# Optimization experiments

Hardware: AMD Instinct MI355X
Metric: run time of the kernel (lower is better)

## Reference

```python
import jax, jax.numpy as jnp
import numpy as np

B, W, F, N = 256, 512, 512, 512


def setup_inputs() -> dict:
    key = jax.random.key(0)
    k1, k2, k3, k4, k5 = jax.random.split(key, 5)
    return {
        "x": jax.random.normal(k1, (B, W, F), dtype=jnp.float32),
        "weight_k": jax.random.normal(k2, (F, N), dtype=jnp.float32),
        "weight_q": jax.random.normal(k3, (F, N), dtype=jnp.float32),
        "weight_v": jax.random.normal(k4, (F, N), dtype=jnp.float32),
        "w": jax.random.normal(k5, (W, 1), dtype=jnp.float32),
    }


def reference(x, weight_k, weight_q, weight_v, w):
    # x: (B, W, F)
    n_outputs = weight_k.shape[-1]
    # Per-word K/V projections (original loops over words; here one batched GEMM)
    K = jnp.einsum("bwf,fn->bwn", x, weight_k)  # (B, W, N)
    V = jnp.einsum("bwf,fn->bwn", x, weight_v)  # (B, W, N)
    # Per-sample query: t = x^T @ w -> (F,), q = t @ weight_q -> (N,)
    t = jnp.einsum("bwf,w->bf", x, w[:, 0])     # (B, F)
    Q = t @ weight_q                              # (B, N)
    # Scores over words, scaled, softmax across the word axis
    scores = jnp.einsum("bn,bwn->bw", Q, K) / jnp.sqrt(jnp.float32(n_outputs))
    weights = jax.nn.softmax(scores, axis=1)      # (B, W)
    # Weighted sum of V over words
    return jnp.einsum("bw,bwn->bn", weights, V)   # (B, N)
```

## Files before the change

kernel.cpp:

```cpp
#include <hip/hip_runtime.h>
#include <math.h>

#define B 256
#define W 512
#define F 512
#define N 512
#define GP 8
#define WPB (W / GP)

__global__ __launch_bounds__(256, 8) void tpart_kernel(
    const float* __restrict__ x,
    const float* __restrict__ wvec,
    float* __restrict__ t_part)
{
    const int blk  = blockIdx.x;
    const int g    = blk & (GP - 1);
    const int b    = blk >> 3;
    const int tid  = threadIdx.x;
    const int half = tid >> 7;
    const int f4   = tid & 127;

    __shared__ float s_w[WPB];
    __shared__ float s_part[2][F];

    if (tid < WPB) s_w[tid] = wvec[g * WPB + tid];
    __syncthreads();

    const float* xb = x + (size_t)b * W * F + (size_t)(g * WPB + half * 32) * F;
    float4 acc = make_float4(0.f, 0.f, 0.f, 0.f);
#pragma unroll 8
    for (int i = 0; i < 32; ++i) {
        const float4 xv = *(const float4*)(xb + (size_t)i * F + f4 * 4);
        const float  ww = s_w[half * 32 + i];
        acc.x += xv.x * ww; acc.y += xv.y * ww;
        acc.z += xv.z * ww; acc.w += xv.w * ww;
    }
    *(float4*)&s_part[half][f4 * 4] = acc;
    __syncthreads();

    t_part[(size_t)blk * F + tid]       = s_part[0][tid]       + s_part[1][tid];
    t_part[(size_t)blk * F + tid + 256] = s_part[0][tid + 256] + s_part[1][tid + 256];
}

__global__ __launch_bounds__(512) void qr_kernel(
    const float* __restrict__ t_part,
    const float* __restrict__ Wq,
    const float* __restrict__ Wk,
    float* __restrict__ r_out)
{
    __shared__ float s_t[F];
    __shared__ float s_q[N];
    const int b = blockIdx.x, tid = threadIdx.x;

    float t = 0.f;
#pragma unroll
    for (int g = 0; g < GP; ++g)
        t += t_part[((size_t)b * GP + g) * F + tid];
    s_t[tid] = t;
    __syncthreads();

    float qa[8] = {0.f, 0.f, 0.f, 0.f, 0.f, 0.f, 0.f, 0.f};
#pragma unroll 4
    for (int f = 0; f < F; f += 8) {
#pragma unroll
        for (int j = 0; j < 8; ++j)
            qa[j] += s_t[f + j] * Wq[(size_t)(f + j) * N + tid];
    }
    s_q[tid] = ((qa[0] + qa[1]) + (qa[2] + qa[3]))
             + ((qa[4] + qa[5]) + (qa[6] + qa[7]));
    __syncthreads();

    const float4* wkrow = (const float4*)(Wk + (size_t)tid * N);
    float r0 = 0.f, r1 = 0.f, r2 = 0.f, r3 = 0.f;
#pragma unroll 8
    for (int n4 = 0; n4 < N / 4; ++n4) {
        const float4 kv = wkrow[n4];
        const float4 qv = *(const float4*)&s_q[n4 * 4];
        r0 += kv.x * qv.x; r1 += kv.y * qv.y;
        r2 += kv.z * qv.z; r3 += kv.w * qv.w;
    }
    r_out[(size_t)b * F + tid] =
        ((r0 + r1) + (r2 + r3)) * 0.04419417382415922f;
}

__global__ __launch_bounds__(256) void attn_part_kernel(
    const float* __restrict__ x,
    const float* __restrict__ r_in,
    float* __restrict__ c_part,
    float* __restrict__ ml_part)
{
    const int blk  = blockIdx.x;
    const int g    = blk & (GP - 1);
    const int b    = blk >> 3;
    const int tid  = threadIdx.x;
    const int lane = tid & 63;
    const int wv   = tid >> 6;

    __shared__ float s_c[4][F];
    __shared__ float s_m[4];
    __shared__ float s_l[4];

    const float* xb = x + (size_t)b * W * F;
    const float* rb = r_in + (size_t)b * F;
    const float4 r0 = *(const float4*)(rb + lane * 4);
    const float4 r1 = *(const float4*)(rb + 256 + lane * 4);

    float m0 = -INFINITY, l0 = 0.f, m1 = -INFINITY, l1 = 0.f;
    float4 cA0 = make_float4(0.f,0.f,0.f,0.f), cA1 = make_float4(0.f,0.f,0.f,0.f);
    float4 cB0 = make_float4(0.f,0.f,0.f,0.f), cB1 = make_float4(0.f,0.f,0.f,0.f);

    const int wbase = g * WPB + wv * 16;
    for (int i = 0; i < 16; i += 4) {
        const float* rA = xb + (size_t)(wbase + i) * F;
        const float* rB = rA + F;
        const float* rC = rB + F;
        const float* rD = rC + F;
        const float4 a0 = *(const float4*)(rA + lane * 4);
        const float4 a1 = *(const float4*)(rA + 256 + lane * 4);
        const float4 b0 = *(const float4*)(rB + lane * 4);
        const float4 b1 = *(const float4*)(rB + 256 + lane * 4);
        const float4 e0 = *(const float4*)(rC + lane * 4);
        const float4 e1 = *(const float4*)(rC + 256 + lane * 4);
        const float4 f0 = *(const float4*)(rD + lane * 4);
        const float4 f1 = *(const float4*)(rD + 256 + lane * 4);

        float dA = a0.x*r0.x + a0.y*r0.y + a0.z*r0.z + a0.w*r0.w
                 + a1.x*r1.x + a1.y*r1.y + a1.z*r1.z + a1.w*r1.w;
        float dB = b0.x*r0.x + b0.y*r0.y + b0.z*r0.z + b0.w*r0.w
                 + b1.x*r1.x + b1.y*r1.y + b1.z*r1.z + b1.w*r1.w;
        float dC = e0.x*r0.x + e0.y*r0.y + e0.z*r0.z + e0.w*r0.w
                 + e1.x*r1.x + e1.y*r1.y + e1.z*r1.z + e1.w*r1.w;
        float dD = f0.x*r0.x + f0.y*r0.y + f0.z*r0.z + f0.w*r0.w
                 + f1.x*r1.x + f1.y*r1.y + f1.z*r1.z + f1.w*r1.w;
#pragma unroll
        for (int off = 32; off >= 1; off >>= 1) {
            dA += __shfl_xor(dA, off, 64);
            dB += __shfl_xor(dB, off, 64);
            dC += __shfl_xor(dC, off, 64);
            dD += __shfl_xor(dD, off, 64);
        }

        {
            float mn = fmaxf(m0, dA);
            float sc = __expf(m0 - mn);
            float p  = __expf(dA - mn);
            l0 = l0 * sc + p;
            cA0.x = cA0.x*sc + p*a0.x; cA0.y = cA0.y*sc + p*a0.y;
            cA0.z = cA0.z*sc + p*a0.z; cA0.w = cA0.w*sc + p*a0.w;
            cA1.x = cA1.x*sc + p*a1.x; cA1.y = cA1.y*sc + p*a1.y;
            cA1.z = cA1.z*sc + p*a1.z; cA1.w = cA1.w*sc + p*a1.w;
            m0 = mn;
            mn = fmaxf(m0, dB);
            sc = __expf(m0 - mn);
            p  = __expf(dB - mn);
            l0 = l0 * sc + p;
            cA0.x = cA0.x*sc + p*b0.x; cA0.y = cA0.y*sc + p*b0.y;
            cA0.z = cA0.z*sc + p*b0.z; cA0.w = cA0.w*sc + p*b0.w;
            cA1.x = cA1.x*sc + p*b1.x; cA1.y = cA1.y*sc + p*b1.y;
            cA1.z = cA1.z*sc + p*b1.z; cA1.w = cA1.w*sc + p*b1.w;
            m0 = mn;
        }
        {
            float mn = fmaxf(m1, dC);
            float sc = __expf(m1 - mn);
            float p  = __expf(dC - mn);
            l1 = l1 * sc + p;
            cB0.x = cB0.x*sc + p*e0.x; cB0.y = cB0.y*sc + p*e0.y;
            cB0.z = cB0.z*sc + p*e0.z; cB0.w = cB0.w*sc + p*e0.w;
            cB1.x = cB1.x*sc + p*e1.x; cB1.y = cB1.y*sc + p*e1.y;
            cB1.z = cB1.z*sc + p*e1.z; cB1.w = cB1.w*sc + p*e1.w;
            m1 = mn;
            mn = fmaxf(m1, dD);
            sc = __expf(m1 - mn);
            p  = __expf(dD - mn);
            l1 = l1 * sc + p;
            cB0.x = cB0.x*sc + p*f0.x; cB0.y = cB0.y*sc + p*f0.y;
            cB0.z = cB0.z*sc + p*f0.z; cB0.w = cB0.w*sc + p*f0.w;
            cB1.x = cB1.x*sc + p*f1.x; cB1.y = cB1.y*sc + p*f1.y;
            cB1.z = cB1.z*sc + p*f1.z; cB1.w = cB1.w*sc + p*f1.w;
            m1 = mn;
        }
    }

    const float Mw = fmaxf(m0, m1);
    const float s0 = __expf(m0 - Mw);
    const float s1 = __expf(m1 - Mw);
    const float Lw = s0 * l0 + s1 * l1;
    float4 w0, w1;
    w0.x = s0*cA0.x + s1*cB0.x; w0.y = s0*cA0.y + s1*cB0.y;
    w0.z = s0*cA0.z + s1*cB0.z; w0.w = s0*cA0.w + s1*cB0.w;
    w1.x = s0*cA1.x + s1*cB1.x; w1.y = s0*cA1.y + s1*cB1.y;
    w1.z = s0*cA1.z + s1*cB1.z; w1.w = s0*cA1.w + s1*cB1.w;

    *(float4*)&s_c[wv][lane * 4]       = w0;
    *(float4*)&s_c[wv][256 + lane * 4] = w1;
    if (lane == 0) { s_m[wv] = Mw; s_l[wv] = Lw; }
    __syncthreads();

    const float M = fmaxf(fmaxf(s_m[0], s_m[1]), fmaxf(s_m[2], s_m[3]));
    const float a0w = __expf(s_m[0] - M), a1w = __expf(s_m[1] - M);
    const float a2w = __expf(s_m[2] - M), a3w = __expf(s_m[3] - M);
    const float L = a0w * s_l[0] + a1w * s_l[1] + a2w * s_l[2] + a3w * s_l[3];

#pragma unroll
    for (int k = 0; k < 2; ++k) {
        const int f = tid + k * 256;
        c_part[(size_t)blk * F + f] =
            a0w * s_c[0][f] + a1w * s_c[1][f] + a2w * s_c[2][f] + a3w * s_c[3][f];
    }
    if (tid == 0) { ml_part[blk * 2] = M; ml_part[blk * 2 + 1] = L; }
}

__global__ __launch_bounds__(512) void combine_kernel(
    const float* __restrict__ c_part,
    const float* __restrict__ ml_part,
    const float* __restrict__ Wv,
    float* __restrict__ out)
{
    __shared__ float s_cf[F];
    const int b = blockIdx.x, tid = threadIdx.x;

    float Mg[GP];
#pragma unroll
    for (int g = 0; g < GP; ++g) Mg[g] = ml_part[(b * GP + g) * 2];
    float M = -INFINITY;
#pragma unroll
    for (int g = 0; g < GP; ++g) M = fmaxf(M, Mg[g]);

    float L = 0.f;
    float alpha[GP];
#pragma unroll
    for (int g = 0; g < GP; ++g) {
        alpha[g] = __expf(Mg[g] - M);
        L += alpha[g] * ml_part[(b * GP + g) * 2 + 1];
    }
    const float invL = 1.f / L;

    float cf = 0.f;
#pragma unroll
    for (int g = 0; g < GP; ++g)
        cf += alpha[g] * c_part[((size_t)b * GP + g) * F + tid];
    s_cf[tid] = cf * invL;
    __syncthreads();

    float oa[8] = {0.f, 0.f, 0.f, 0.f, 0.f, 0.f, 0.f, 0.f};
#pragma unroll 4
    for (int f = 0; f < F; f += 8) {
#pragma unroll
        for (int j = 0; j < 8; ++j)
            oa[j] += s_cf[f + j] * Wv[(size_t)(f + j) * N + tid];
    }
    out[(size_t)b * N + tid] = ((oa[0] + oa[1]) + (oa[2] + oa[3]))
                             + ((oa[4] + oa[5]) + (oa[6] + oa[7]));
}

extern "C" void kernel_launch(void* const* d_in, const int* in_sizes, int n_in,
                              void* d_out, int out_size, void* d_ws, size_t ws_size,
                              hipStream_t stream)
{
    const float* x    = (const float*)d_in[0];
    const float* Wk   = (const float*)d_in[1];
    const float* Wq   = (const float*)d_in[2];
    const float* Wv   = (const float*)d_in[3];
    const float* wvec = (const float*)d_in[4];
    float* out     = (float*)d_out;
    float* t_part  = (float*)d_ws;
    float* r       = t_part + (size_t)B * GP * F;
    float* c_part  = r + (size_t)B * F;
    float* ml_part = c_part + (size_t)B * GP * F;

    tpart_kernel<<<B * GP, 256, 0, stream>>>(x, wvec, t_part);
    qr_kernel<<<B, 512, 0, stream>>>(t_part, Wq, Wk, r);
    attn_part_kernel<<<B * GP, 256, 0, stream>>>(x, r, c_part, ml_part);
    combine_kernel<<<B, 512, 0, stream>>>(c_part, ml_part, Wv, out);
}
```

Measured before the change: 495.0 us.

## Fuse four kernels into one persistent kernel with software grid barriers

Replaces the four separate launches with a single kernel of 512 blocks that moves between phases using atomic-counter grid barriers. It also cuts the word-split factor from 8 to 2, so each block handles more words and the Q, r and output projections are split across the two blocks of a batch. The goal is to remove launch gaps and partial-reduction traffic. The risks are much lower parallelism during the x-streaming phases and deadlock if all 512 blocks are not co-resident, since no cooperative launch is used.

```diff
diff --git a/kernel.cpp b/kernel.cpp
--- a/kernel.cpp
+++ b/kernel.cpp
@@ -5,253 +5,279 @@
 #define W 512
 #define F 512
 #define N 512
-#define GP 8
+#define GP 2
+#define NBLK (B * GP)
 #define WPB (W / GP)
 
-__global__ __launch_bounds__(256, 8) void tpart_kernel(
+__device__ inline void grid_barrier(unsigned* cnt, unsigned* gen) {
+    __syncthreads();
+    if (threadIdx.x == 0) {
+        __threadfence();
+        unsigned g = __hip_atomic_load(gen, __ATOMIC_RELAXED, __HIP_MEMORY_SCOPE_AGENT);
+        unsigned arrived = __hip_atomic_fetch_add(cnt, 1u, __ATOMIC_ACQ_REL, __HIP_MEMORY_SCOPE_AGENT);
+        if (arrived == NBLK - 1) {
+            __hip_atomic_store(cnt, 0u, __ATOMIC_RELAXED, __HIP_MEMORY_SCOPE_AGENT);
+            __hip_atomic_store(gen, g + 1u, __ATOMIC_RELEASE, __HIP_MEMORY_SCOPE_AGENT);
+        } else {
+            while (__hip_atomic_load(gen, __ATOMIC_ACQUIRE, __HIP_MEMORY_SCOPE_AGENT) == g) {
+                __builtin_amdgcn_s_sleep(2);
+            }
+        }
+        __threadfence();
+    }
+    __syncthreads();
+}
+
+__global__ void init_barrier(unsigned* bar) {
+    bar[0] = 0u;
+    bar[1] = 0u;
+}
+
+__global__ __launch_bounds__(256, 4) void fused_kernel(
     const float* __restrict__ x,
+    const float* __restrict__ Wk,
+    const float* __restrict__ Wq,
+    const float* __restrict__ Wv,
     const float* __restrict__ wvec,
-    float* __restrict__ t_part)
-{
-    const int blk  = blockIdx.x;
-    const int g    = blk & (GP - 1);
-    const int b    = blk >> 3;
-    const int tid  = threadIdx.x;
-    const int half = tid >> 7;
-    const int f4   = tid & 127;
-
-    __shared__ float s_w[WPB];
-    __shared__ float s_part[2][F];
-
-    if (tid < WPB) s_w[tid] = wvec[g * WPB + tid];
-    __syncthreads();
-
-    const float* xb = x + (size_t)b * W * F + (size_t)(g * WPB + half * 32) * F;
-    float4 acc = make_float4(0.f, 0.f, 0.f, 0.f);
-#pragma unroll 8
-    for (int i = 0; i < 32; ++i) {
-        const float4 xv = *(const float4*)(xb + (size_t)i * F + f4 * 4);
-        const float  ww = s_w[half * 32 + i];
-        acc.x += xv.x * ww; acc.y += xv.y * ww;
-        acc.z += xv.z * ww; acc.w += xv.w * ww;
-    }
-    *(float4*)&s_part[half][f4 * 4] = acc;
-    __syncthreads();
-
-    t_part[(size_t)blk * F + tid]       = s_part[0][tid]       + s_part[1][tid];
-    t_part[(size_t)blk * F + tid + 256] = s_part[0][tid + 256] + s_part[1][tid + 256];
-}
-
-__global__ __launch_bounds__(512) void qr_kernel(
-    const float* __restrict__ t_part,
-    const float* __restrict__ Wq,
-    const float* __restrict__ Wk,
-    float* __restrict__ r_out)
-{
-    __shared__ float s_t[F];
-    __shared__ float s_q[N];
-    const int b = blockIdx.x, tid = threadIdx.x;
-
-    float t = 0.f;
-#pragma unroll
-    for (int g = 0; g < GP; ++g)
-        t += t_part[((size_t)b * GP + g) * F + tid];
-    s_t[tid] = t;
-    __syncthreads();
-
-    float qa[8] = {0.f, 0.f, 0.f, 0.f, 0.f, 0.f, 0.f, 0.f};
-#pragma unroll 4
-    for (int f = 0; f < F; f += 8) {
-#pragma unroll
-        for (int j = 0; j < 8; ++j)
-            qa[j] += s_t[f + j] * Wq[(size_t)(f + j) * N + tid];
-    }
-    s_q[tid] = ((qa[0] + qa[1]) + (qa[2] + qa[3]))
-             + ((qa[4] + qa[5]) + (qa[6] + qa[7]));
-    __syncthreads();
-
-    const float4* wkrow = (const float4*)(Wk + (size_t)tid * N);
-    float r0 = 0.f, r1 = 0.f, r2 = 0.f, r3 = 0.f;
-#pragma unroll 8
-    for (int n4 = 0; n4 < N / 4; ++n4) {
-        const float4 kv = wkrow[n4];
-        const float4 qv = *(const float4*)&s_q[n4 * 4];
-        r0 += kv.x * qv.x; r1 += kv.y * qv.y;
-        r2 += kv.z * qv.z; r3 += kv.w * qv.w;
-    }
-    r_out[(size_t)b * F + tid] =
-        ((r0 + r1) + (r2 + r3)) * 0.04419417382415922f;
-}
-
-__global__ __launch_bounds__(256) void attn_part_kernel(
-    const float* __restrict__ x,
-    const float* __restrict__ r_in,
+    unsigned*    __restrict__ bar,
+    float* __restrict__ t_part,
+    float* __restrict__ Qbuf,
+    float* __restrict__ rbuf,
     float* __restrict__ c_part,
-    float* __restrict__ ml_part)
-{
-    const int blk  = blockIdx.x;
-    const int g    = blk & (GP - 1);
-    const int b    = blk >> 3;
-    const int tid  = threadIdx.x;
-    const int lane = tid & 63;
-    const int wv   = tid >> 6;
-
-    __shared__ float s_c[4][F];
-    __shared__ float s_m[4];
-    __shared__ float s_l[4];
-
-    const float* xb = x + (size_t)b * W * F;
-    const float* rb = r_in + (size_t)b * F;
-    const float4 r0 = *(const float4*)(rb + lane * 4);
-    const float4 r1 = *(const float4*)(rb + 256 + lane * 4);
-
-    float m0 = -INFINITY, l0 = 0.f, m1 = -INFINITY, l1 = 0.f;
-    float4 cA0 = make_float4(0.f,0.f,0.f,0.f), cA1 = make_float4(0.f,0.f,0.f,0.f);
-    float4 cB0 = make_float4(0.f,0.f,0.f,0.f), cB1 = make_float4(0.f,0.f,0.f,0.f);
-
-    const int wbase = g * WPB + wv * 16;
-    for (int i = 0; i < 16; i += 4) {
-        const float* rA = xb + (size_t)(wbase + i) * F;
-        const float* rB = rA + F;
-        const float* rC = rB + F;
-        const float* rD = rC + F;
-        const float4 a0 = *(const float4*)(rA + lane * 4);
-        const float4 a1 = *(const float4*)(rA + 256 + lane * 4);
-        const float4 b0 = *(const float4*)(rB + lane * 4);
-        const float4 b1 = *(const float4*)(rB + 256 + lane * 4);
-        const float4 e0 = *(const float4*)(rC + lane * 4);
-        const float4 e1 = *(const float4*)(rC + 256 + lane * 4);
-        const float4 f0 = *(const float4*)(rD + lane * 4);
-        const float4 f1 = *(const float4*)(rD + 256 + lane * 4);
-
-        float dA = a0.x*r0.x + a0.y*r0.y + a0.z*r0.z + a0.w*r0.w
-                 + a1.x*r1.x + a1.y*r1.y + a1.z*r1.z + a1.w*r1.w;
-        float dB = b0.x*r0.x + b0.y*r0.y + b0.z*r0.z + b0.w*r0.w
-                 + b1.x*r1.x + b1.y*r1.y + b1.z*r1.z + b1.w*r1.w;
-        float dC = e0.x*r0.x + e0.y*r0.y + e0.z*r0.z + e0.w*r0.w
-                 + e1.x*r1.x + e1.y*r1.y + e1.z*r1.z + e1.w*r1.w;
-        float dD = f0.x*r0.x + f0.y*r0.y + f0.z*r0.z + f0.w*r0.w
-                 + f1.x*r1.x + f1.y*r1.y + f1.z*r1.z + f1.w*r1.w;
-#pragma unroll
-        for (int off = 32; off >= 1; off >>= 1) {
-            dA += __shfl_xor(dA, off, 64);
-            dB += __shfl_xor(dB, off, 64);
-            dC += __shfl_xor(dC, off, 64);
-            dD += __shfl_xor(dD, off, 64);
-        }
-
-        {
-            float mn = fmaxf(m0, dA);
-            float sc = __expf(m0 - mn);
-            float p  = __expf(dA - mn);
-            l0 = l0 * sc + p;
-            cA0.x = cA0.x*sc + p*a0.x; cA0.y = cA0.y*sc + p*a0.y;
-            cA0.z = cA0.z*sc + p*a0.z; cA0.w = cA0.w*sc + p*a0.w;
-            cA1.x = cA1.x*sc + p*a1.x; cA1.y = cA1.y*sc + p*a1.y;
-            cA1.z = cA1.z*sc + p*a1.z; cA1.w = cA1.w*sc + p*a1.w;
-            m0 = mn;
-            mn = fmaxf(m0, dB);
-            sc = __expf(m0 - mn);
-            p  = __expf(dB - mn);
-            l0 = l0 * sc + p;
-            cA0.x = cA0.x*sc + p*b0.x; cA0.y = cA0.y*sc + p*b0.y;
-            cA0.z = cA0.z*sc + p*b0.z; cA0.w = cA0.w*sc + p*b0.w;
-            cA1.x = cA1.x*sc + p*b1.x; cA1.y = cA1.y*sc + p*b1.y;
-            cA1.z = cA1.z*sc + p*b1.z; cA1.w = cA1.w*sc + p*b1.w;
-            m0 = mn;
-        }
-        {
-            float mn = fmaxf(m1, dC);
-            float sc = __expf(m1 - mn);
-            float p  = __expf(dC - mn);
-            l1 = l1 * sc + p;
-            cB0.x = cB0.x*sc + p*e0.x; cB0.y = cB0.y*sc + p*e0.y;
-            cB0.z = cB0.z*sc + p*e0.z; cB0.w = cB0.w*sc + p*e0.w;
-            cB1.x = cB1.x*sc + p*e1.x; cB1.y = cB1.y*sc + p*e1.y;
-            cB1.z = cB1.z*sc + p*e1.z; cB1.w = cB1.w*sc + p*e1.w;
-            m1 = mn;
-            mn = fmaxf(m1, dD);
-            sc = __expf(m1 - mn);
-            p  = __expf(dD - mn);
-            l1 = l1 * sc + p;
-            cB0.x = cB0.x*sc + p*f0.x; cB0.y = cB0.y*sc + p*f0.y;
-            cB0.z = cB0.z*sc + p*f0.z; cB0.w = cB0.w*sc + p*f0.w;
-            cB1.x = cB1.x*sc + p*f1.x; cB1.y = cB1.y*sc + p*f1.y;
-            cB1.z = cB1.z*sc + p*f1.z; cB1.w = cB1.w*sc + p*f1.w;
-            m1 = mn;
-        }
-    }
-
-    const float Mw = fmaxf(m0, m1);
-    const float s0 = __expf(m0 - Mw);
-    const float s1 = __expf(m1 - Mw);
-    const float Lw = s0 * l0 + s1 * l1;
-    float4 w0, w1;
-    w0.x = s0*cA0.x + s1*cB0.x; w0.y = s0*cA0.y + s1*cB0.y;
-    w0.z = s0*cA0.z + s1*cB0.z; w0.w = s0*cA0.w + s1*cB0.w;
-    w1.x = s0*cA1.x + s1*cB1.x; w1.y = s0*cA1.y + s1*cB1.y;
-    w1.z = s0*cA1.z + s1*cB1.z; w1.w = s0*cA1.w + s1*cB1.w;
-
-    *(float4*)&s_c[wv][lane * 4]       = w0;
-    *(float4*)&s_c[wv][256 + lane * 4] = w1;
-    if (lane == 0) { s_m[wv] = Mw; s_l[wv] = Lw; }
-    __syncthreads();
-
-    const float M = fmaxf(fmaxf(s_m[0], s_m[1]), fmaxf(s_m[2], s_m[3]));
-    const float a0w = __expf(s_m[0] - M), a1w = __expf(s_m[1] - M);
-    const float a2w = __expf(s_m[2] - M), a3w = __expf(s_m[3] - M);
-    const float L = a0w * s_l[0] + a1w * s_l[1] + a2w * s_l[2] + a3w * s_l[3];
-
-#pragma unroll
-    for (int k = 0; k < 2; ++k) {
-        const int f = tid + k * 256;
-        c_part[(size_t)blk * F + f] =
-            a0w * s_c[0][f] + a1w * s_c[1][f] + a2w * s_c[2][f] + a3w * s_c[3][f];
-    }
-    if (tid == 0) { ml_part[blk * 2] = M; ml_part[blk * 2 + 1] = L; }
-}
-
-__global__ __launch_bounds__(512) void combine_kernel(
-    const float* __restrict__ c_part,
-    const float* __restrict__ ml_part,
-    const float* __restrict__ Wv,
+    float* __restrict__ ml_part,
     float* __restrict__ out)
 {
-    __shared__ float s_cf[F];
-    const int b = blockIdx.x, tid = threadIdx.x;
-
-    float Mg[GP];
-#pragma unroll
-    for (int g = 0; g < GP; ++g) Mg[g] = ml_part[(b * GP + g) * 2];
-    float M = -INFINITY;
-#pragma unroll
-    for (int g = 0; g < GP; ++g) M = fmaxf(M, Mg[g]);
-
-    float L = 0.f;
-    float alpha[GP];
-#pragma unroll
-    for (int g = 0; g < GP; ++g) {
-        alpha[g] = __expf(Mg[g] - M);
-        L += alpha[g] * ml_part[(b * GP + g) * 2 + 1];
-    }
-    const float invL = 1.f / L;
-
-    float cf = 0.f;
-#pragma unroll
-    for (int g = 0; g < GP; ++g)
-        cf += alpha[g] * c_part[((size_t)b * GP + g) * F + tid];
-    s_cf[tid] = cf * invL;
-    __syncthreads();
-
-    float oa[8] = {0.f, 0.f, 0.f, 0.f, 0.f, 0.f, 0.f, 0.f};
-#pragma unroll 4
-    for (int f = 0; f < F; f += 8) {
-#pragma unroll
-        for (int j = 0; j < 8; ++j)
-            oa[j] += s_cf[f + j] * Wv[(size_t)(f + j) * N + tid];
-    }
-    out[(size_t)b * N + tid] = ((oa[0] + oa[1]) + (oa[2] + oa[3]))
-                             + ((oa[4] + oa[5]) + (oa[6] + oa[7]));
+    const int blk = blockIdx.x;
+    const int g   = blk & (GP - 1);
+    const int b   = blk >> 1;
+    const int tid = threadIdx.x;
+
+    __shared__ float smem[2056];
+
+    unsigned* cnt = bar;
+    unsigned* gen = bar + 1;
+
+    {
+        float* s_w    = smem;
+        float* s_part = smem + 256;
+        s_w[tid] = wvec[g * WPB + tid];
+        __syncthreads();
+
+        const int half = tid >> 7;
+        const int f4   = tid & 127;
+        const float* xb = x + (size_t)b * W * F + (size_t)(g * WPB + half * 128) * F;
+
+        float4 acc = make_float4(0.f, 0.f, 0.f, 0.f);
+        for (int c = 0; c < 16; ++c) {
+            float wr[8];
+#pragma unroll
+            for (int j = 0; j < 8; ++j) wr[j] = s_w[half * 128 + c * 8 + j];
+            float4 xv[8];
+#pragma unroll
+            for (int j = 0; j < 8; ++j)
+                xv[j] = *(const float4*)(xb + (size_t)(c * 8 + j) * F + f4 * 4);
+#pragma unroll
+            for (int j = 0; j < 8; ++j) {
+                acc.x += xv[j].x * wr[j]; acc.y += xv[j].y * wr[j];
+                acc.z += xv[j].z * wr[j]; acc.w += xv[j].w * wr[j];
+            }
+        }
+        *(float4*)&s_part[half * 512 + f4 * 4] = acc;
+        __syncthreads();
+
+        t_part[(size_t)blk * F + tid]       = s_part[tid]       + s_part[512 + tid];
+        t_part[(size_t)blk * F + tid + 256] = s_part[tid + 256] + s_part[768 + tid];
+    }
+    grid_barrier(cnt, gen);
+
+    {
+        float* s_t = smem;
+        const float* tp0 = t_part + ((size_t)b * GP + 0) * F;
+        const float* tp1 = t_part + ((size_t)b * GP + 1) * F;
+        s_t[tid]       = tp0[tid]       + tp1[tid];
+        s_t[tid + 256] = tp0[tid + 256] + tp1[tid + 256];
+        __syncthreads();
+
+        const float* wqc = Wq + g * 256 + tid;
+        float qa[8] = {0.f,0.f,0.f,0.f,0.f,0.f,0.f,0.f};
+        for (int f = 0; f < F; f += 8) {
+#pragma unroll
+            for (int j = 0; j < 8; ++j)
+                qa[j] += s_t[f + j] * wqc[(size_t)(f + j) * N];
+        }
+        Qbuf[(size_t)b * N + g * 256 + tid] =
+            ((qa[0]+qa[1])+(qa[2]+qa[3])) + ((qa[4]+qa[5])+(qa[6]+qa[7]));
+    }
+    grid_barrier(cnt, gen);
+
+    {
+        float* s_q = smem;
+        s_q[tid]       = Qbuf[(size_t)b * N + tid];
+        s_q[tid + 256] = Qbuf[(size_t)b * N + tid + 256];
+        __syncthreads();
+
+        const int ff = g * 256 + tid;
+        const float4* krow = (const float4*)(Wk + (size_t)ff * N);
+        const float4* qv4  = (const float4*)s_q;
+        float ra[4] = {0.f, 0.f, 0.f, 0.f};
+#pragma unroll 8
+        for (int n4 = 0; n4 < N / 4; ++n4) {
+            const float4 kv = krow[n4];
+            const float4 qv = qv4[n4];
+            ra[0] += kv.x * qv.x; ra[1] += kv.y * qv.y;
+            ra[2] += kv.z * qv.z; ra[3] += kv.w * qv.w;
+        }
+        rbuf[(size_t)b * F + ff] =
+            ((ra[0] + ra[1]) + (ra[2] + ra[3])) * 0.04419417382415922f;
+    }
+    grid_barrier(cnt, gen);
+
+    {
+        float* s_c = smem;
+        float* s_m = smem + 2048;
+        float* s_l = smem + 2052;
+        const int lane = tid & 63;
+        const int wv   = tid >> 6;
+
+        const float* xb = x + (size_t)b * W * F;
+        const float* rb = rbuf + (size_t)b * F;
+        const float4 r0 = *(const float4*)(rb + lane * 4);
+        const float4 r1 = *(const float4*)(rb + 256 + lane * 4);
+
+        float m0 = -INFINITY, l0 = 0.f, m1 = -INFINITY, l1 = 0.f;
+        float4 cA0 = make_float4(0.f,0.f,0.f,0.f), cA1 = make_float4(0.f,0.f,0.f,0.f);
+        float4 cB0 = make_float4(0.f,0.f,0.f,0.f), cB1 = make_float4(0.f,0.f,0.f,0.f);
+
+        const int wbase = g * WPB + wv * 64;
+        for (int i = 0; i < 64; i += 4) {
+            const float* rA = xb + (size_t)(wbase + i) * F;
+            const float* rB = rA + F;
+            const float* rC = rB + F;
+            const float* rD = rC + F;
+            const float4 a0 = *(const float4*)(rA + lane * 4);
+            const float4 a1 = *(const float4*)(rA + 256 + lane * 4);
+            const float4 b0 = *(const float4*)(rB + lane * 4);
+            const float4 b1 = *(const float4*)(rB + 256 + lane * 4);
+            const float4 e0 = *(const float4*)(rC + lane * 4);
+            const float4 e1 = *(const float4*)(rC + 256 + lane * 4);
+            const float4 f0 = *(const float4*)(rD + lane * 4);
+            const float4 f1 = *(const float4*)(rD + 256 + lane * 4);
+
+            float dA = a0.x*r0.x + a0.y*r0.y + a0.z*r0.z + a0.w*r0.w
+                     + a1.x*r1.x + a1.y*r1.y + a1.z*r1.z + a1.w*r1.w;
+            float dB = b0.x*r0.x + b0.y*r0.y + b0.z*r0.z + b0.w*r0.w
+                     + b1.x*r1.x + b1.y*r1.y + b1.z*r1.z + b1.w*r1.w;
+            float dC = e0.x*r0.x + e0.y*r0.y + e0.z*r0.z + e0.w*r0.w
+                     + e1.x*r1.x + e1.y*r1.y + e1.z*r1.z + e1.w*r1.w;
+            float dD = f0.x*r0.x + f0.y*r0.y + f0.z*r0.z + f0.w*r0.w
+                     + f1.x*r1.x + f1.y*r1.y + f1.z*r1.z + f1.w*r1.w;
+#pragma unroll
+            for (int off = 32; off >= 1; off >>= 1) {
+                dA += __shfl_xor(dA, off, 64);
+                dB += __shfl_xor(dB, off, 64);
+                dC += __shfl_xor(dC, off, 64);
+                dD += __shfl_xor(dD, off, 64);
+            }
+
+            {
+                float mn = fmaxf(m0, dA);
+                float sc = __expf(m0 - mn);
+                float p  = __expf(dA - mn);
+                l0 = l0 * sc + p;
+                cA0.x = cA0.x*sc + p*a0.x; cA0.y = cA0.y*sc + p*a0.y;
+                cA0.z = cA0.z*sc + p*a0.z; cA0.w = cA0.w*sc + p*a0.w;
+                cA1.x = cA1.x*sc + p*a1.x; cA1.y = cA1.y*sc + p*a1.y;
+                cA1.z = cA1.z*sc + p*a1.z; cA1.w = cA1.w*sc + p*a1.w;
+                m0 = mn;
+                mn = fmaxf(m0, dB);
+                sc = __expf(m0 - mn);
+                p  = __expf(dB - mn);
+                l0 = l0 * sc + p;
+                cA0.x = cA0.x*sc + p*b0.x; cA0.y = cA0.y*sc + p*b0.y;
+                cA0.z = cA0.z*sc + p*b0.z; cA0.w = cA0.w*sc + p*b0.w;
+                cA1.x = cA1.x*sc + p*b1.x; cA1.y = cA1.y*sc + p*b1.y;
+                cA1.z = cA1.z*sc + p*b1.z; cA1.w = cA1.w*sc + p*b1.w;
+                m0 = mn;
+            }
+            {
+                float mn = fmaxf(m1, dC);
+                float sc = __expf(m1 - mn);
+                float p  = __expf(dC - mn);
+                l1 = l1 * sc + p;
+                cB0.x = cB0.x*sc + p*e0.x; cB0.y = cB0.y*sc + p*e0.y;
+                cB0.z = cB0.z*sc + p*e0.z; cB0.w = cB0.w*sc + p*e0.w;
+                cB1.x = cB1.x*sc + p*e1.x; cB1.y = cB1.y*sc + p*e1.y;
+                cB1.z = cB1.z*sc + p*e1.z; cB1.w = cB1.w*sc + p*e1.w;
+                m1 = mn;
+                mn = fmaxf(m1, dD);
+                sc = __expf(m1 - mn);
+                p  = __expf(dD - mn);
+                l1 = l1 * sc + p;
+                cB0.x = cB0.x*sc + p*f0.x; cB0.y = cB0.y*sc + p*f0.y;
+                cB0.z = cB0.z*sc + p*f0.z; cB0.w = cB0.w*sc + p*f0.w;
+                cB1.x = cB1.x*sc + p*f1.x; cB1.y = cB1.y*sc + p*f1.y;
+                cB1.z = cB1.z*sc + p*f1.z; cB1.w = cB1.w*sc + p*f1.w;
+                m1 = mn;
+            }
+        }
+
+        const float Mw = fmaxf(m0, m1);
+        const float s0 = __expf(m0 - Mw);
+        const float s1 = __expf(m1 - Mw);
+        const float Lw = s0 * l0 + s1 * l1;
+        float4 w0, w1;
+        w0.x = s0*cA0.x + s1*cB0.x; w0.y = s0*cA0.y + s1*cB0.y;
+        w0.z = s0*cA0.z + s1*cB0.z; w0.w = s0*cA0.w + s1*cB0.w;
+        w1.x = s0*cA1.x + s1*cB1.x; w1.y = s0*cA1.y + s1*cB1.y;
+        w1.z = s0*cA1.z + s1*cB1.z; w1.w = s0*cA1.w + s1*cB1.w;
+
+        *(float4*)&s_c[wv * 512 + lane * 4]       = w0;
+        *(float4*)&s_c[wv * 512 + 256 + lane * 4] = w1;
+        if (lane == 0) { s_m[wv] = Mw; s_l[wv] = Lw; }
+        __syncthreads();
+
+        const float M = fmaxf(fmaxf(s_m[0], s_m[1]), fmaxf(s_m[2], s_m[3]));
+        const float a0w = __expf(s_m[0] - M), a1w = __expf(s_m[1] - M);
+        const float a2w = __expf(s_m[2] - M), a3w = __expf(s_m[3] - M);
+        const float L = a0w*s_l[0] + a1w*s_l[1] + a2w*s_l[2] + a3w*s_l[3];
+
+#pragma unroll
+        for (int k = 0; k < 2; ++k) {
+            const int f = tid + k * 256;
+            c_part[(size_t)blk * F + f] =
+                a0w*s_c[f] + a1w*s_c[512+f] + a2w*s_c[1024+f] + a3w*s_c[1536+f];
+        }
+        if (tid == 0) { ml_part[blk * 2] = M; ml_part[blk * 2 + 1] = L; }
+    }
+    grid_barrier(cnt, gen);
+
+    {
+        float* s_cf = smem;
+        const float M0 = ml_part[(b * GP + 0) * 2];
+        const float M1 = ml_part[(b * GP + 1) * 2];
+        const float M  = fmaxf(M0, M1);
+        const float a0 = __expf(M0 - M);
+        const float a1 = __expf(M1 - M);
+        const float L  = a0 * ml_part[(b * GP + 0) * 2 + 1]
+                       + a1 * ml_part[(b * GP + 1) * 2 + 1];
+        const float invL = 1.f / L;
+
+        const float* cp0 = c_part + ((size_t)b * GP + 0) * F;
+        const float* cp1 = c_part + ((size_t)b * GP + 1) * F;
+        s_cf[tid]       = (a0 * cp0[tid]       + a1 * cp1[tid])       * invL;
+        s_cf[tid + 256] = (a0 * cp0[tid + 256] + a1 * cp1[tid + 256]) * invL;
+        __syncthreads();
+
+        const float* wvc = Wv + g * 256 + tid;
+        float oa[8] = {0.f,0.f,0.f,0.f,0.f,0.f,0.f,0.f};
+        for (int f = 0; f < F; f += 8) {
+#pragma unroll
+            for (int j = 0; j < 8; ++j)
+                oa[j] += s_cf[f + j] * wvc[(size_t)(f + j) * N];
+        }
+        out[(size_t)b * N + g * 256 + tid] =
+            ((oa[0]+oa[1])+(oa[2]+oa[3])) + ((oa[4]+oa[5])+(oa[6]+oa[7]));
+    }
 }
 
 extern "C" void kernel_launch(void* const* d_in, const int* in_sizes, int n_in,
@@ -263,14 +289,16 @@
     const float* Wq   = (const float*)d_in[2];
     const float* Wv   = (const float*)d_in[3];
     const float* wvec = (const float*)d_in[4];
-    float* out     = (float*)d_out;
-    float* t_part  = (float*)d_ws;
-    float* r       = t_part + (size_t)B * GP * F;
-    float* c_part  = r + (size_t)B * F;
-    float* ml_part = c_part + (size_t)B * GP * F;
-
-    tpart_kernel<<<B * GP, 256, 0, stream>>>(x, wvec, t_part);
-    qr_kernel<<<B, 512, 0, stream>>>(t_part, Wq, Wk, r);
-    attn_part_kernel<<<B * GP, 256, 0, stream>>>(x, r, c_part, ml_part);
-    combine_kernel<<<B, 512, 0, stream>>>(c_part, ml_part, Wv, out);
+    float* out = (float*)d_out;
+
+    unsigned* bar  = (unsigned*)d_ws;
+    float* t_part  = (float*)d_ws + 64;
+    float* Qbuf    = t_part + (size_t)NBLK * F;
+    float* rbuf    = Qbuf + (size_t)B * N;
+    float* c_part  = rbuf + (size_t)B * F;
+    float* ml_part = c_part + (size_t)NBLK * F;
+
+    init_barrier<<<1, 1, 0, stream>>>(bar);
+    fused_kernel<<<NBLK, 256, 0, stream>>>(x, Wk, Wq, Wv, wvec, bar,
+                                           t_part, Qbuf, rbuf, c_part, ml_part, out);
 }
```

Measured after the change: 814.0 us. 64.4% more time.
